# Optimization experiments

Measured on AMD Instinct MI355X. Metric: run time of the kernel, lower is better.

## Reference

```python
import jax, jax.numpy as jnp
import numpy as np

N_NODES = 50000
N_EDGES = 500000
F_IN = 128
HID = 160      # hidden_sf * model_dim = 5 * 32
F_OUT = 128    # out_sf * output_channels = 4 * 32
N_GRAPHS = 50
OUT_DIM = 10


def setup_inputs() -> dict:
    key = jax.random.key(0)
    ks = jax.random.split(key, 16)
    x = jax.random.normal(ks[0], (N_NODES, F_IN), dtype=jnp.float32)
    edge_index = jax.random.randint(ks[1], (2, N_EDGES), 0, N_NODES, dtype=jnp.int64)
    batch = jnp.sort(jax.random.randint(ks[2], (N_NODES,), 0, N_GRAPHS, dtype=jnp.int64))

    def lin(k, fi, fo):
        return jax.random.normal(k, (fi, fo), dtype=jnp.float32) * (1.0 / np.sqrt(fi))

    dims = [(F_IN, HID), (HID, HID), (HID, HID), (HID, F_OUT)]
    params = {}
    for i, (fi, fo) in enumerate(dims):
        params[f"W{i}"] = lin(ks[3 + i], fi, fo)
        params[f"b{i}"] = jnp.zeros((fo,), dtype=jnp.float32)
    params["fc_w"] = lin(ks[8], F_OUT, OUT_DIM)
    params["fc_b"] = jnp.zeros((OUT_DIM,), dtype=jnp.float32)
    return {"x": x, "edge_index": edge_index, "batch": batch, **params}


def _gcn_layer(x, W, b, src, dst, dinv):
    # PyG GCNConv (improved=True): x' = D^{-1/2}(A + 2I)D^{-1/2} X W + b
    xw = x @ W                                   # [N, F_out]
    norm = dinv[src] * dinv[dst]                 # [E]
    msgs = xw[src] * norm[:, None]               # [E, F_out] gather
    agg = jax.ops.segment_sum(msgs, dst, num_segments=N_NODES)  # scatter-add
    # self-loop contribution with fill value 2 (improved)
    agg = agg + (2.0 * dinv * dinv)[:, None] * xw
    return agg + b


def reference(x, edge_index, batch, W0, b0, W1, b1, W2, b2, W3, b3, fc_w, fc_b):
    src, dst = edge_index[0], edge_index[1]
    ones_e = jnp.ones((N_EDGES,), dtype=x.dtype)
    deg = jax.ops.segment_sum(ones_e, dst, num_segments=N_NODES) + 2.0
    dinv = jax.lax.rsqrt(deg)

    h = x
    for (W, b) in [(W0, b0), (W1, b1), (W2, b2), (W3, b3)]:
        h = _gcn_layer(h, W, b, src, dst, dinv)

    # global mean pool per graph
    sums = jax.ops.segment_sum(h, batch, num_segments=N_GRAPHS)        # [G, F_OUT]
    cnts = jax.ops.segment_sum(jnp.ones((N_NODES,), h.dtype), batch, num_segments=N_GRAPHS)
    pooled = sums / jnp.maximum(cnts, 1.0)[:, None]

    logits = pooled @ fc_w + fc_b
    return jax.nn.log_softmax(logits, axis=1)
```

## Files before the change

kernel.cpp:

```cpp
#include <hip/hip_runtime.h>

#define N_NODES 50000
#define N_EDGES 500000
#define F_IN    128
#define HID     160
#define NG      50
#define OUT_DIM 10
#define PC      16
#define MAXDEG  48
#define PADK    164
#define FSTRIDE 132

#define NRANGE  8
#define RNODES  (N_NODES / NRANGE)
#define FILLB   128
#define FB      (NRANGE * FILLB)
#define NPACK   (N_EDGES / 4)

#define XF_ROWS   32
#define XF_BLOCKS ((N_NODES + XF_ROWS - 1) / XF_ROWS)
#define ZERO_BLOCKS ((N_NODES + 1023) / 1024)

__global__ __launch_bounds__(1024)
void k_init(const float* __restrict__ W0, const float* __restrict__ b0,
            const float* __restrict__ W1, const float* __restrict__ b1,
            const float* __restrict__ W2, const float* __restrict__ b2,
            const float* __restrict__ W3, const float* __restrict__ b3,
            const float* __restrict__ fcw, const int* __restrict__ batch,
            float* __restrict__ Fmt, float* __restrict__ r0,
            float* __restrict__ r1, float* __restrict__ r2,
            float* __restrict__ r3, int* __restrict__ start,
            int* __restrict__ deg) {
    const int t = threadIdx.x;
    if (blockIdx.x >= 2) {
        int i = (blockIdx.x - 2) * 1024 + t;
        if (i < N_NODES) deg[i] = 0;
        return;
    }
    if (blockIdx.x == 1) {
        int g = t;
        if (g > NG) return;
        int lo = 0, hi = N_NODES;
        while (lo < hi) {
            int mid = (lo + hi) >> 1;
            if (batch[mid] < g) lo = mid + 1; else hi = mid;
        }
        start[g] = lo;
        return;
    }
    __shared__ float sA[OUT_DIM * PADK];
    __shared__ float sB[OUT_DIM * PADK];
    float* cur = sA;
    float* nxt = sB;

    for (int idx = t; idx < F_IN * OUT_DIM; idx += 1024) {
        int k = idx / OUT_DIM, c = idx - k * OUT_DIM;
        cur[c * PADK + k] = fcw[idx];
    }
    __syncthreads();
    if (t < OUT_DIM) {
        float acc = 0.f;
        const float4* Bv = (const float4*)b3;
        for (int k4 = 0; k4 < F_IN / 4; ++k4) {
            float4 w = Bv[k4];
            float4 b = *(const float4*)&cur[t * PADK + 4 * k4];
            acc += w.x * b.x + w.y * b.y + w.z * b.z + w.w * b.w;
        }
        r3[t] = acc;
    }

    const int r = t >> 2, q = t & 3;
    auto stage = [&](const float* __restrict__ W, const float* __restrict__ bias,
                     float* __restrict__ biasOut, int M, int K, bool toGlobal) {
        const bool isBias = (r == M) && (bias != nullptr);
        const bool active = (r < M) || isBias;
        float acc[OUT_DIM];
        #pragma unroll
        for (int c = 0; c < OUT_DIM; ++c) acc[c] = 0.f;
        if (active) {
            const float* Arow = isBias ? bias : (W + r * K);
            const float4* Wv = (const float4*)Arow;
            const int nit = K >> 4;
            #pragma unroll 2
            for (int it = 0; it < nit; ++it) {
                float4 w = Wv[it * 4 + q];
                #pragma unroll
                for (int c = 0; c < OUT_DIM; ++c) {
                    float4 b = *(const float4*)&cur[c * PADK + it * 16 + q * 4];
                    acc[c] += w.x * b.x + w.y * b.y + w.z * b.z + w.w * b.w;
                }
            }
        }
        #pragma unroll
        for (int c = 0; c < OUT_DIM; ++c) {
            acc[c] += __shfl_xor(acc[c], 1);
            acc[c] += __shfl_xor(acc[c], 2);
        }
        if (active && q == 0) {
            if (isBias) {
                #pragma unroll
                for (int c = 0; c < OUT_DIM; ++c) biasOut[c] = acc[c];
            } else if (toGlobal) {
                #pragma unroll
                for (int c = 0; c < OUT_DIM; ++c) Fmt[c * FSTRIDE + r] = acc[c];
            } else {
                #pragma unroll
                for (int c = 0; c < OUT_DIM; ++c) nxt[c * PADK + r] = acc[c];
            }
        }
        __syncthreads();
        float* tmp = cur; cur = nxt; nxt = tmp;
    };

    stage(W3, nullptr, nullptr, HID, F_IN, false);
    stage(W2, b2, r2, HID, HID, false);
    stage(W1, b1, r1, HID, HID, false);
    stage(W0, b0, r0, F_IN, HID, true);
}

__global__ void k_fill_xf(const int* __restrict__ src, const int* __restrict__ dst,
                          int* __restrict__ deg, int* __restrict__ ell,
                          const float* __restrict__ X, const float* __restrict__ Fmt,
                          float* __restrict__ Y0) {
    const int t = threadIdx.x;
    if (blockIdx.x < FB) {
        const int rb    = blockIdx.x;
        const int range = rb & (NRANGE - 1);
        const int sub   = rb >> 3;
        const int lo    = range * RNODES;
        const int4* d4 = (const int4*)dst;
        const int4* s4 = (const int4*)src;
        for (int pk = sub * 256 + t; pk < NPACK; pk += FILLB * 256) {
            const int4 dv = d4[pk];
            const int4 sv = s4[pk];
            #pragma unroll
            for (int j = 0; j < 4; ++j) {
                const int d = (&dv.x)[j];
                if ((unsigned)(d - lo) < (unsigned)RNODES) {
                    int p = atomicAdd(&deg[d], 1);
                    if (p < MAXDEG) ell[d * MAXDEG + p] = (&sv.x)[j];
                }
            }
        }
        return;
    }
    __shared__ float sX[XF_ROWS][132];
    __shared__ float sFt[OUT_DIM * FSTRIDE];
    const int base = (blockIdx.x - FB) * XF_ROWS;
    for (int idx = t; idx < XF_ROWS * F_IN; idx += 256) {
        int rr = idx >> 7, kk = idx & 127;
        int gr = base + rr;
        sX[rr][kk] = (gr < N_NODES) ? X[(size_t)gr * F_IN + kk] : 0.f;
    }
    for (int idx = t; idx < OUT_DIM * FSTRIDE; idx += 256) sFt[idx] = Fmt[idx];
    __syncthreads();
    const int r = t >> 4, c = t & 15;
    float a0 = 0.f, a1 = 0.f;
    if (c < OUT_DIM) {
        for (int k = 0; k < F_IN; k += 4) {
            const float4 x0 = *(const float4*)&sX[r][k];
            const float4 x1 = *(const float4*)&sX[r + 16][k];
            const float4 f  = *(const float4*)&sFt[c * FSTRIDE + k];
            a0 += x0.x * f.x + x0.y * f.y + x0.z * f.z + x0.w * f.w;
            a1 += x1.x * f.x + x1.y * f.y + x1.z * f.z + x1.w * f.w;
        }
    }
    const float pad = (c == 10) ? 1.0f : 0.0f;
    const float v0 = (c < OUT_DIM) ? a0 : pad;
    const float v1 = (c < OUT_DIM) ? a1 : pad;
    const int g0 = base + r, g1 = base + r + 16;
    if (g0 < N_NODES) Y0[(size_t)g0 * PC + c] = v0;
    if (g1 < N_NODES) Y0[(size_t)g1 * PC + c] = v1;
}

__global__ void k_prop16(const float* __restrict__ in, const int* __restrict__ deg,
                         const int* __restrict__ ell, float* __restrict__ out) {
    const int gid  = blockIdx.x * blockDim.x + threadIdx.x;
    const int i    = gid >> 6;
    const int lane = threadIdx.x & 63;
    const int esub = lane >> 4, c = lane & 15;
    const int d = deg[i];
    const int dc = (d < MAXDEG) ? d : MAXDEG;
    float acc = 0.f;
    const int base = i * MAXDEG;
    for (int k = esub; k < dc; k += 4) {
        int s = ell[base + k];
        float ds = rsqrtf((float)deg[s] + 2.0f);
        acc += ds * in[(size_t)s * PC + c];
    }
    acc += __shfl_xor(acc, 16);
    acc += __shfl_xor(acc, 32);
    if (lane < 16) {
        float di = rsqrtf((float)d + 2.0f);
        out[(size_t)i * PC + c] = di * (acc + 2.0f * di * in[(size_t)i * PC + c]);
    }
}

__global__ void k_pool_final(const float* __restrict__ Y1, const float* __restrict__ Y2,
                             const float* __restrict__ Y3, const float* __restrict__ Y4,
                             const int* __restrict__ start,
                             const float* __restrict__ r0, const float* __restrict__ r1,
                             const float* __restrict__ r2, const float* __restrict__ r3,
                             const float* __restrict__ fcb, float* __restrict__ out) {
    const int g = blockIdx.x, t = threadIdx.x;
    __shared__ float red[256];
    __shared__ float S_sh[16];
    __shared__ float qsh[3];
    __shared__ float lg[OUT_DIM];
    const int st = start[g], cnt = start[g + 1] - st;
    const int c = t & 15, rr = t >> 4;

    float acc = 0.f;
    for (int r = rr; r < cnt; r += 16) acc += Y4[(size_t)(st + r) * PC + c];
    red[t] = acc; __syncthreads();
    if (t < 128) red[t] += red[t + 128]; __syncthreads();
    if (t < 64)  red[t] += red[t + 64];  __syncthreads();
    if (t < 32)  red[t] += red[t + 32];  __syncthreads();
    if (t < 16)  S_sh[t] = red[t] + red[t + 16];

    float a1 = 0.f, a2 = 0.f, a3 = 0.f;
    for (int r = t; r < cnt; r += 256) {
        a1 += Y1[(size_t)(st + r) * PC + 10];
        a2 += Y2[(size_t)(st + r) * PC + 10];
        a3 += Y3[(size_t)(st + r) * PC + 10];
    }
    __syncthreads(); red[t] = a1; __syncthreads();
    for (int o = 128; o > 0; o >>= 1) { if (t < o) red[t] += red[t + o]; __syncthreads(); }
    if (t == 0) qsh[0] = red[0];
    __syncthreads(); red[t] = a2; __syncthreads();
    for (int o = 128; o > 0; o >>= 1) { if (t < o) red[t] += red[t + o]; __syncthreads(); }
    if (t == 0) qsh[1] = red[0];
    __syncthreads(); red[t] = a3; __syncthreads();
    for (int o = 128; o > 0; o >>= 1) { if (t < o) red[t] += red[t + o]; __syncthreads(); }
    if (t == 0) qsh[2] = red[0];
    __syncthreads();

    if (t < OUT_DIM) {
        float n = (float)cnt; if (n < 1.f) n = 1.f;
        lg[t] = (S_sh[t] + qsh[2] * r0[t] + qsh[1] * r1[t] + qsh[0] * r2[t]) / n
                + r3[t] + fcb[t];
    }
    __syncthreads();
    if (t == 0) {
        float m = -1e30f;
        for (int o = 0; o < OUT_DIM; ++o) m = fmaxf(m, lg[o]);
        float ss = 0.f;
        for (int o = 0; o < OUT_DIM; ++o) ss += expf(lg[o] - m);
        float ls = logf(ss) + m;
        for (int o = 0; o < OUT_DIM; ++o) out[g * OUT_DIM + o] = lg[o] - ls;
    }
}

extern "C" void kernel_launch(void* const* d_in, const int* in_sizes, int n_in,
                              void* d_out, int out_size, void* d_ws, size_t ws_size,
                              hipStream_t stream) {
    const float* x     = (const float*)d_in[0];
    const int*   ei    = (const int*)d_in[1];
    const int*   src   = ei;
    const int*   dstp  = ei + N_EDGES;
    const int*   batch = (const int*)d_in[2];
    const float* W0 = (const float*)d_in[3];
    const float* b0 = (const float*)d_in[4];
    const float* W1 = (const float*)d_in[5];
    const float* b1 = (const float*)d_in[6];
    const float* W2 = (const float*)d_in[7];
    const float* b2 = (const float*)d_in[8];
    const float* W3 = (const float*)d_in[9];
    const float* b3 = (const float*)d_in[10];
    const float* fcw = (const float*)d_in[11];
    const float* fcb = (const float*)d_in[12];
    float* out = (float*)d_out;

    char* p = (char*)d_ws;
    auto alloc = [&](size_t bytes) -> void* {
        void* r = (void*)p;
        p += (bytes + 255) & ~(size_t)255;
        return r;
    };
    int*   deg   = (int*)alloc(N_NODES * 4);
    int*   start = (int*)alloc((NG + 1) * 4);
    int*   ell   = (int*)alloc((size_t)N_NODES * MAXDEG * 4);
    float* Fmt   = (float*)alloc(OUT_DIM * FSTRIDE * 4);
    float* r0    = (float*)alloc(OUT_DIM * 4);
    float* r1    = (float*)alloc(OUT_DIM * 4);
    float* r2    = (float*)alloc(OUT_DIM * 4);
    float* r3    = (float*)alloc(OUT_DIM * 4);
    float* Y0    = (float*)alloc((size_t)N_NODES * PC * 4);
    float* Y1    = (float*)alloc((size_t)N_NODES * PC * 4);
    float* Y2    = (float*)alloc((size_t)N_NODES * PC * 4);
    float* Y3    = (float*)alloc((size_t)N_NODES * PC * 4);
    float* Y4    = (float*)alloc((size_t)N_NODES * PC * 4);

    const int TB = 256;
    k_init<<<ZERO_BLOCKS + 2, 1024, 0, stream>>>(W0, b0, W1, b1, W2, b2, W3, b3,
                                                 fcw, batch, Fmt, r0, r1, r2, r3,
                                                 start, deg);
    k_fill_xf<<<FB + XF_BLOCKS, TB, 0, stream>>>(src, dstp, deg, ell, x, Fmt, Y0);

    const int PROP_BLOCKS = N_NODES * 64 / TB;
    k_prop16<<<PROP_BLOCKS, TB, 0, stream>>>(Y0, deg, ell, Y1);
    k_prop16<<<PROP_BLOCKS, TB, 0, stream>>>(Y1, deg, ell, Y2);
    k_prop16<<<PROP_BLOCKS, TB, 0, stream>>>(Y2, deg, ell, Y3);
    k_prop16<<<PROP_BLOCKS, TB, 0, stream>>>(Y3, deg, ell, Y4);

    k_pool_final<<<NG, TB, 0, stream>>>(Y1, Y2, Y3, Y4, start, r0, r1, r2, r3, fcb, out);
}
```

Measured before the change: 241.8 us.

## Prescale propagation by D^-1/2 and store ELL indices as 16-bit

The middle propagation layers now carry D^{-1/2}-scaled features (Z = D^{-1/2} Y). Three of the four prop kernels therefore no longer gather deg[s] or compute an rsqrt per edge. Pooling rebuilds the unscaled values by multiplying by sqrt(deg+2). The ELL neighbour list is also stored as unsigned short, which halves index traffic; this depends on the node count staying below 65536. The cost is slightly different floating-point rounding and a new per-node deg read in the pool kernel.

```diff
diff --git a/kernel.cpp b/kernel.cpp
--- a/kernel.cpp
+++ b/kernel.cpp
@@ -119,7 +119,7 @@
 }
 
 __global__ void k_fill_xf(const int* __restrict__ src, const int* __restrict__ dst,
-                          int* __restrict__ deg, int* __restrict__ ell,
+                          int* __restrict__ deg, unsigned short* __restrict__ ell,
                           const float* __restrict__ X, const float* __restrict__ Fmt,
                           float* __restrict__ Y0) {
     const int t = threadIdx.x;
@@ -138,7 +138,7 @@
                 const int d = (&dv.x)[j];
                 if ((unsigned)(d - lo) < (unsigned)RNODES) {
                     int p = atomicAdd(&deg[d], 1);
-                    if (p < MAXDEG) ell[d * MAXDEG + p] = (&sv.x)[j];
+                    if (p < MAXDEG) ell[d * MAXDEG + p] = (unsigned short)(&sv.x)[j];
                 }
             }
         }
@@ -173,8 +173,9 @@
     if (g1 < N_NODES) Y0[(size_t)g1 * PC + c] = v1;
 }
 
+template<int MODE>
 __global__ void k_prop16(const float* __restrict__ in, const int* __restrict__ deg,
-                         const int* __restrict__ ell, float* __restrict__ out) {
+                         const unsigned short* __restrict__ ell, float* __restrict__ out) {
     const int gid  = blockIdx.x * blockDim.x + threadIdx.x;
     const int i    = gid >> 6;
     const int lane = threadIdx.x & 63;
@@ -185,20 +186,25 @@
     const int base = i * MAXDEG;
     for (int k = esub; k < dc; k += 4) {
         int s = ell[base + k];
-        float ds = rsqrtf((float)deg[s] + 2.0f);
-        acc += ds * in[(size_t)s * PC + c];
+        if (MODE == 0) acc += rsqrtf((float)deg[s] + 2.0f) * in[(size_t)s * PC + c];
+        else           acc += in[(size_t)s * PC + c];
     }
     acc += __shfl_xor(acc, 16);
     acc += __shfl_xor(acc, 32);
     if (lane < 16) {
-        float di = rsqrtf((float)d + 2.0f);
-        out[(size_t)i * PC + c] = di * (acc + 2.0f * di * in[(size_t)i * PC + c]);
-    }
-}
-
-__global__ void k_pool_final(const float* __restrict__ Y1, const float* __restrict__ Y2,
-                             const float* __restrict__ Y3, const float* __restrict__ Y4,
-                             const int* __restrict__ start,
+        const float self = in[(size_t)i * PC + c];
+        const float dp2 = (float)d + 2.0f;
+        float o;
+        if (MODE == 0)      o = (acc + 2.0f * rsqrtf(dp2) * self) / dp2;
+        else if (MODE == 1) o = (acc + 2.0f * self) / dp2;
+        else                o = (acc + 2.0f * self) * rsqrtf(dp2);
+        out[(size_t)i * PC + c] = o;
+    }
+}
+
+__global__ void k_pool_final(const float* __restrict__ Z1, const float* __restrict__ Z2,
+                             const float* __restrict__ Z3, const float* __restrict__ Y4,
+                             const int* __restrict__ start, const int* __restrict__ deg,
                              const float* __restrict__ r0, const float* __restrict__ r1,
                              const float* __restrict__ r2, const float* __restrict__ r3,
                              const float* __restrict__ fcb, float* __restrict__ out) {
@@ -220,9 +226,10 @@
 
     float a1 = 0.f, a2 = 0.f, a3 = 0.f;
     for (int r = t; r < cnt; r += 256) {
-        a1 += Y1[(size_t)(st + r) * PC + 10];
-        a2 += Y2[(size_t)(st + r) * PC + 10];
-        a3 += Y3[(size_t)(st + r) * PC + 10];
+        const float sq = sqrtf((float)deg[st + r] + 2.0f);
+        a1 += sq * Z1[(size_t)(st + r) * PC + 10];
+        a2 += sq * Z2[(size_t)(st + r) * PC + 10];
+        a3 += sq * Z3[(size_t)(st + r) * PC + 10];
     }
     __syncthreads(); red[t] = a1; __syncthreads();
     for (int o = 128; o > 0; o >>= 1) { if (t < o) red[t] += red[t + o]; __syncthreads(); }
@@ -277,18 +284,18 @@
         p += (bytes + 255) & ~(size_t)255;
         return r;
     };
-    int*   deg   = (int*)alloc(N_NODES * 4);
-    int*   start = (int*)alloc((NG + 1) * 4);
-    int*   ell   = (int*)alloc((size_t)N_NODES * MAXDEG * 4);
+    int*            deg   = (int*)alloc(N_NODES * 4);
+    int*            start = (int*)alloc((NG + 1) * 4);
+    unsigned short* ell   = (unsigned short*)alloc((size_t)N_NODES * MAXDEG * 2);
     float* Fmt   = (float*)alloc(OUT_DIM * FSTRIDE * 4);
     float* r0    = (float*)alloc(OUT_DIM * 4);
     float* r1    = (float*)alloc(OUT_DIM * 4);
     float* r2    = (float*)alloc(OUT_DIM * 4);
     float* r3    = (float*)alloc(OUT_DIM * 4);
     float* Y0    = (float*)alloc((size_t)N_NODES * PC * 4);
-    float* Y1    = (float*)alloc((size_t)N_NODES * PC * 4);
-    float* Y2    = (float*)alloc((size_t)N_NODES * PC * 4);
-    float* Y3    = (float*)alloc((size_t)N_NODES * PC * 4);
+    float* Z1    = (float*)alloc((size_t)N_NODES * PC * 4);
+    float* Z2    = (float*)alloc((size_t)N_NODES * PC * 4);
+    float* Z3    = (float*)alloc((size_t)N_NODES * PC * 4);
     float* Y4    = (float*)alloc((size_t)N_NODES * PC * 4);
 
     const int TB = 256;
@@ -298,10 +305,11 @@
     k_fill_xf<<<FB + XF_BLOCKS, TB, 0, stream>>>(src, dstp, deg, ell, x, Fmt, Y0);
 
     const int PROP_BLOCKS = N_NODES * 64 / TB;
-    k_prop16<<<PROP_BLOCKS, TB, 0, stream>>>(Y0, deg, ell, Y1);
-    k_prop16<<<PROP_BLOCKS, TB, 0, stream>>>(Y1, deg, ell, Y2);
-    k_prop16<<<PROP_BLOCKS, TB, 0, stream>>>(Y2, deg, ell, Y3);
-    k_prop16<<<PROP_BLOCKS, TB, 0, stream>>>(Y3, deg, ell, Y4);
-
-    k_pool_final<<<NG, TB, 0, stream>>>(Y1, Y2, Y3, Y4, start, r0, r1, r2, r3, fcb, out);
-}
+    k_prop16<0><<<PROP_BLOCKS, TB, 0, stream>>>(Y0, deg, ell, Z1);
+    k_prop16<1><<<PROP_BLOCKS, TB, 0, stream>>>(Z1, deg, ell, Z2);
+    k_prop16<1><<<PROP_BLOCKS, TB, 0, stream>>>(Z2, deg, ell, Z3);
+    k_prop16<2><<<PROP_BLOCKS, TB, 0, stream>>>(Z3, deg, ell, Y4);
+
+    k_pool_final<<<NG, TB, 0, stream>>>(Z1, Z2, Z3, Y4, start, deg,
+                                        r0, r1, r2, r3, fcb, out);
+}
```

After: 238.9 us. No clear change (-1.2%).
